# Performance work log

Hardware: AMD Instinct MI355X
Metric: run time of the kernel (lower is better)

The kernel has to match this reference:

```python
import jax, jax.numpy as jnp
import numpy as np

N_NODES = 50000


def _degrees(idx, n):
    d = jax.ops.segment_sum(jnp.ones(idx.shape, jnp.float32), idx, num_segments=n)
    return jnp.clip(d, 1.0)  # DGL clamps degree at 1


def gcn_layer(x, src, dst, W, b, n):
    """DGL GraphConv with norm='both': D_dst^-1/2 * sum_edges(D_src^-1/2 * x_src) @ W + b.
    Applies W before aggregation when in_feats > out_feats (cheaper), matching DGL."""
    inv_sqrt_out = _degrees(src, n) ** -0.5  # out-degree norm on source side
    inv_sqrt_in = _degrees(dst, n) ** -0.5   # in-degree norm on dest side
    h = x * inv_sqrt_out[:, None]
    if W.shape[0] > W.shape[1]:
        h = h @ W
        agg = jax.ops.segment_sum(h[src], dst, num_segments=n)
    else:
        agg = jax.ops.segment_sum(h[src], dst, num_segments=n)
        agg = agg @ W
    return agg * inv_sqrt_in[:, None] + b


def setup_inputs() -> dict:
    key = jax.random.key(0)
    ks = jax.random.split(key, 8)
    E = 800000
    in_feat = jax.random.normal(ks[0], (N_NODES, 1), dtype=jnp.float32)
    edge_index = jax.random.randint(ks[1], (2, E), 0, N_NODES, dtype=jnp.int32)
    def glorot(k, fan_in, fan_out):
        s = (6.0 / (fan_in + fan_out)) ** 0.5
        return jax.random.uniform(k, (fan_in, fan_out), jnp.float32, -s, s)
    W0 = glorot(ks[2], 1, 100); b0 = jnp.zeros((100,), jnp.float32)
    W1 = glorot(ks[3], 100, 10); b1 = jnp.zeros((10,), jnp.float32)
    W2 = glorot(ks[4], 10, 1); b2 = jnp.zeros((1,), jnp.float32)
    return {"in_feat": in_feat, "edge_index": edge_index,
            "W0": W0, "b0": b0, "W1": W1, "b1": b1, "W2": W2, "b2": b2}


def reference(in_feat, edge_index, W0, b0, W1, b1, W2, b2):
    src, dst = edge_index[0], edge_index[1]
    n = N_NODES
    h = gcn_layer(in_feat, src, dst, W0, b0, n)
    h = jax.nn.leaky_relu(h, negative_slope=0.01)
    h = gcn_layer(h, src, dst, W1, b1, n)
    h = jax.nn.relu(h)
    h = gcn_layer(h, src, dst, W2, b2, n)
    h = jax.nn.relu(h)
    return h
```

## Files before the change

kernel.cpp:

```cpp
#include <hip/hip_runtime.h>


#define NT 256
#define NTB 1024
#define K_BKT 250
#define R_NODES 200
#define SEG 48
#define CAP 4096
#define CHUNK 4096
#define BIN_BLOCKS 196
#define NSLOT (BIN_BLOCKS * SEG)
#define FINF 3.0e38f


__global__ __launch_bounds__(NT) void k_bin(const int4* __restrict__ src4,
                                            const int4* __restrict__ dst4, int E4,
                                            unsigned short* __restrict__ cntd16,
                                            unsigned short* __restrict__ cnts16,
                                            unsigned* __restrict__ dstSeg,
                                            unsigned short* __restrict__ srcSeg) {
  __shared__ unsigned cnt_d[K_BKT], cnt_s[K_BKT];
  int t = threadIdx.x, blk = blockIdx.x;
  for (int k = t; k < K_BKT; k += NT) { cnt_d[k] = 0u; cnt_s[k] = 0u; }
  __syncthreads();
  int base4 = blk * (CHUNK / 4);
  int4 sA[4], dA[4];
#pragma unroll
  for (int j = 0; j < 4; j++) {
    int e4 = base4 + j * NT + t;
    if (e4 < E4) { sA[j] = src4[e4]; dA[j] = dst4[e4]; }
    else { sA[j] = make_int4(-1, -1, -1, -1); dA[j] = make_int4(-1, -1, -1, -1); }
  }
  const int* sp = (const int*)sA;
  const int* dp = (const int*)dA;
#pragma unroll
  for (int j = 0; j < 16; j++) {
    int d = dp[j], s = sp[j];
    if (d >= 0) {
      unsigned bd = (unsigned)d / R_NODES;
      unsigned pd = atomicAdd(&cnt_d[bd], 1u);
      if (pd < SEG)
        dstSeg[((size_t)bd * BIN_BLOCKS + blk) * SEG + pd] =
            (unsigned)s | (((unsigned)d - bd * R_NODES) << 16);
      unsigned bs = (unsigned)s / R_NODES;
      unsigned ps = atomicAdd(&cnt_s[bs], 1u);
      if (ps < SEG)
        srcSeg[((size_t)bs * BIN_BLOCKS + blk) * SEG + ps] =
            (unsigned short)((unsigned)s - bs * R_NODES);
    }
  }
  __syncthreads();
  for (int k = t; k < K_BKT; k += NT) {
    unsigned cd = cnt_d[k]; if (cd > SEG) cd = SEG;
    unsigned cs = cnt_s[k]; if (cs > SEG) cs = SEG;
    cntd16[(size_t)blk * K_BKT + k] = (unsigned short)cd;
    cnts16[(size_t)blk * K_BKT + k] = (unsigned short)cs;
  }
}


struct BktLds {
  unsigned dslab[NSLOT];
  unsigned short sslab[NSLOT];
  unsigned cnt[R_NODES], cnts[R_NODES], cur[R_NODES];
  unsigned sc[256];
  unsigned short crow_d[256], crow_s[256];
  unsigned short stage[CAP];
};
struct PreLds {
  float W0s[100], b0s[100], W1s[1000];
  float beta[100], bsorted[128];
  int ord[100];
  float cA[1000], cB[1000];
  float baseA[16], baseB[16];
};
union BPool { BktLds b; PreLds p; };

__global__ __launch_bounds__(NTB) void k_bucket(
    const unsigned short* __restrict__ cntd16, const unsigned short* __restrict__ cnts16,
    const unsigned* __restrict__ dstSeg, const unsigned short* __restrict__ srcSeg,
    const float* __restrict__ x,
    const float* __restrict__ W0, const float* __restrict__ b0,
    const float* __restrict__ W1,
    float* __restrict__ betas, float* __restrict__ Aseg, float* __restrict__ Bseg,
    unsigned short* __restrict__ csr16,
    unsigned* __restrict__ rs, unsigned* __restrict__ rd,
    float* __restrict__ dsrc_inv, float* __restrict__ ddst_inv,
    float* __restrict__ s0, int n, int nbin) {
  __shared__ BPool u;
  int t = threadIdx.x, blk = blockIdx.x;
  if (blk < K_BKT) {
    const int b = blk;
    const int4* dsl4 = (const int4*)(dstSeg + (size_t)b * NSLOT);
    int4* dl4 = (int4*)u.b.dslab;
    for (int i = t; i < NSLOT / 4; i += NTB) dl4[i] = dsl4[i];
    const int4* ssl4 = (const int4*)(srcSeg + (size_t)b * NSLOT);
    int4* sl4 = (int4*)u.b.sslab;
    for (int i = t; i < NSLOT / 8; i += NTB) sl4[i] = ssl4[i];
    if (t < 256) {
      u.b.crow_d[t] = (t < nbin) ? cntd16[(size_t)t * K_BKT + b] : (unsigned short)0;
      u.b.crow_s[t] = (t < nbin) ? cnts16[(size_t)t * K_BKT + b] : (unsigned short)0;
    }
    for (int k = t; k < R_NODES; k += NTB) { u.b.cnt[k] = 0u; u.b.cnts[k] = 0u; }
    __syncthreads();
    for (int sl = t; sl < NSLOT; sl += NTB) {
      int blkI = sl / SEG, idx = sl - blkI * SEG;
      if (idx < (int)u.b.crow_d[blkI]) atomicAdd(&u.b.cnt[u.b.dslab[sl] >> 16], 1u);
      if (idx < (int)u.b.crow_s[blkI]) atomicAdd(&u.b.cnts[u.b.sslab[sl]], 1u);
    }
    __syncthreads();
    unsigned v = 0u;
    if (t < 256) {
      v = (t < R_NODES) ? u.b.cnt[t] : 0u;
      u.b.sc[t] = v;
    }
    __syncthreads();
    for (int off = 1; off < 256; off <<= 1) {
      unsigned a = (t >= off && t < 256) ? u.b.sc[t - off] : 0u;
      __syncthreads();
      if (t < 256) u.b.sc[t] += a;
      __syncthreads();
    }
    if (t < R_NODES) {
      unsigned st = u.b.sc[t] - v;
      int vg = b * R_NODES + t;
      if (vg < n) {
        unsigned di = u.b.cnt[t], dou = u.b.cnts[t];
        rs[vg] = (unsigned)b * CAP + st;
        rd[vg] = di;
        ddst_inv[vg] = rsqrtf((float)(di < 1u ? 1u : di));
        float ia = rsqrtf((float)(dou < 1u ? 1u : dou));
        dsrc_inv[vg] = ia;
        s0[vg] = x[vg] * ia;
      }
      u.b.cur[t] = st;
    }
    __syncthreads();
    for (int sl = t; sl < NSLOT; sl += NTB) {
      int blkI = sl / SEG, idx = sl - blkI * SEG;
      if (idx < (int)u.b.crow_d[blkI]) {
        unsigned e = u.b.dslab[sl];
        unsigned pos = atomicAdd(&u.b.cur[e >> 16], 1u);
        if (pos < CAP) u.b.stage[pos] = (unsigned short)(e & 0xFFFFu);
      }
    }
    __syncthreads();
    unsigned nd = u.b.sc[255]; if (nd > CAP) nd = CAP;
    int4* cg4 = (int4*)(csr16 + (size_t)b * CAP);
    const int4* st4 = (const int4*)u.b.stage;
    unsigned nv = (nd + 7) / 8;
    for (unsigned i = t; i < nv; i += NTB) cg4[i] = st4[i];
  } else {
    if (t < 100) { u.p.W0s[t] = W0[t]; u.p.b0s[t] = b0[t]; }
    for (int k = t; k < 1000; k += NTB) u.p.W1s[k] = W1[k];
    __syncthreads();
    if (t < 100) {
      float w = u.p.W0s[t];
      u.p.beta[t] = (w != 0.0f) ? (-u.p.b0s[t] / w) : FINF;
    }
    __syncthreads();
    if (t < 100) {
      float bt = u.p.beta[t];
      int r = 0;
      for (int j = 0; j < 100; j++) {
        float bj = u.p.beta[j];
        r += (bj < bt || (bj == bt && j < t)) ? 1 : 0;
      }
      u.p.bsorted[r] = bt;
      u.p.ord[r] = t;
    }
    if (t >= 100 && t < 128) u.p.bsorted[t] = FINF;
    __syncthreads();
    if (t < 128) betas[t] = u.p.bsorted[t];
    if (t < 1000) {
      int k = t / 10, j = t - k * 10;
      int f = u.p.ord[k];
      float w = u.p.W0s[f];
      float w1 = u.p.W1s[f * 10 + j];
      float ca = 0.0f, cb = 0.0f;
      if (w != 0.0f) {
        ca = 0.99f * fabsf(w) * w1;
        cb = 0.99f * ((w > 0.0f) ? 1.0f : -1.0f) * u.p.b0s[f] * w1;
      }
      u.p.cA[t] = ca;
      u.p.cB[t] = cb;
    }
    if (t < 10) {
      const int j = t;
      float a = 0.0f, bacc = 0.0f;
      for (int f = 0; f < 100; f++) {
        float w = u.p.W0s[f], bb = u.p.b0s[f], w1 = u.p.W1s[f * 10 + j];
        if (w == 0.0f) {
          float h = bb >= 0.0f ? bb : 0.01f * bb;
          bacc += h * w1;
        } else {
          float cc = (w > 0.0f) ? 0.01f : 1.0f;
          a += cc * w * w1;
          bacc += cc * bb * w1;
        }
      }
      Aseg[j] = a; Bseg[j] = bacc;
      u.p.baseA[j] = a; u.p.baseB[j] = bacc;
    }
    __syncthreads();
    for (int off = 1; off < 100; off <<= 1) {
      float a = 0.0f, bv = 0.0f;
      bool act = (t < 1000) && (t / 10 >= off);
      if (act) { a = u.p.cA[t - off * 10]; bv = u.p.cB[t - off * 10]; }
      __syncthreads();
      if (act) { u.p.cA[t] += a; u.p.cB[t] += bv; }
      __syncthreads();
    }
    if (t < 1000) {
      int k = t / 10, j = t - k * 10;
      Aseg[(k + 1) * 10 + j] = u.p.baseA[j] + u.p.cA[t];
      Bseg[(k + 1) * 10 + j] = u.p.baseB[j] + u.p.cB[t];
    }
  }
}


__global__ void k_g_l0l1(const unsigned* __restrict__ rs, const unsigned* __restrict__ rd,
                         const unsigned short* __restrict__ csr16,
                         const float* __restrict__ s0,
                         const float* __restrict__ dsrc_inv, const float* __restrict__ ddst_inv,
                         const float* __restrict__ betas,
                         float4* __restrict__ y4, int n) {
  __shared__ float bs_[128];
  for (int k = threadIdx.x; k < 128; k += blockDim.x) bs_[k] = betas[k];
  __syncthreads();
  int tid = blockIdx.x * blockDim.x + threadIdx.x;
  int v = tid >> 2, k4 = tid & 3;
  if (v >= n) return;
  unsigned base = rs[v], deg = rd[v];
  const unsigned short* row = csr16 + base;
  float c = 0.0f;
#pragma unroll 4
  for (unsigned i = k4; i < deg; i += 4) c += s0[row[i]];
  c += __shfl_xor(c, 1, 4);
  c += __shfl_xor(c, 2, 4);
  float c0 = c * ddst_inv[v];
  int lo = 0, hi = 100;
#pragma unroll
  for (int it = 0; it < 7; it++) {
    int mid = (lo + hi) >> 1;
    bool go = bs_[mid] < c0;
    lo = go ? mid + 1 : lo;
    hi = go ? hi : mid;
  }
  if (k4 == 0) {
    float so = dsrc_inv[v];
    y4[v] = make_float4(so * c0, so, __int_as_float(lo), 0.0f);
  }
}

__global__ void k_g10_l1l2(const unsigned* __restrict__ rs, const unsigned* __restrict__ rd,
                           const unsigned short* __restrict__ csr16,
                           const float4* __restrict__ y4,
                           const float* __restrict__ dsrc_inv, const float* __restrict__ ddst_inv,
                           const float* __restrict__ Aseg, const float* __restrict__ Bseg,
                           const float* __restrict__ b1, const float* __restrict__ W2,
                           float* __restrict__ t2, int n) {
  __shared__ float As[1010], Bs[1010];
  for (int k = threadIdx.x; k < 1010; k += blockDim.x) { As[k] = Aseg[k]; Bs[k] = Bseg[k]; }
  __syncthreads();
  int tid = blockIdx.x * blockDim.x + threadIdx.x;
  int v = tid >> 4, f = tid & 15;
  if (v >= n) return;
  unsigned base = rs[v], deg = rd[v];
  const unsigned short* row = csr16 + base;
  float acc = 0.0f;
  for (unsigned c = 0; c < deg; c += 16u) {
    unsigned i = c + (unsigned)f;
    int idx = (i < deg) ? (int)row[i] : 0;
    float4 y = y4[idx];
    unsigned m = deg - c; if (m > 16u) m = 16u;
    for (unsigned j = 0; j < m; j++) {
      float soc = __shfl(y.x, (int)j, 16);
      float so = __shfl(y.y, (int)j, 16);
      int sg = __shfl(__float_as_int(y.z), (int)j, 16);
      if (f < 10) {
        int o = sg * 10 + f;
        acc = fmaf(soc, As[o], acc);
        acc = fmaf(so, Bs[o], acc);
      }
    }
  }
  float p = 0.0f;
  if (f < 10) {
    float h = acc * ddst_inv[v] + b1[f];
    h = h > 0.0f ? h : 0.0f;
    p = h * W2[f];
  }
  p += __shfl_xor(p, 1, 16);
  p += __shfl_xor(p, 2, 16);
  p += __shfl_xor(p, 4, 16);
  p += __shfl_xor(p, 8, 16);
  if (f == 0) t2[v] = p * dsrc_inv[v];
}

__global__ void k_g_out(const unsigned* __restrict__ rs, const unsigned* __restrict__ rd,
                        const unsigned short* __restrict__ csr16,
                        const float* __restrict__ t2, const float* __restrict__ ddst_inv,
                        const float* __restrict__ b2, float* __restrict__ out, int n) {
  int tid = blockIdx.x * blockDim.x + threadIdx.x;
  int v = tid >> 2, k4 = tid & 3;
  if (v >= n) return;
  unsigned base = rs[v], deg = rd[v];
  const unsigned short* row = csr16 + base;
  float c = 0.0f;
#pragma unroll 4
  for (unsigned i = k4; i < deg; i += 4) c += t2[row[i]];
  c += __shfl_xor(c, 1, 4);
  c += __shfl_xor(c, 2, 4);
  if (k4 == 0) {
    float h = c * ddst_inv[v] + b2[0];
    out[v] = h > 0.0f ? h : 0.0f;
  }
}

extern "C" void kernel_launch(void* const* d_in, const int* in_sizes, int n_in,
                              void* d_out, int out_size, void* d_ws, size_t ws_size,
                              hipStream_t stream) {
  const float* in_feat = (const float*)d_in[0];
  const int* ei = (const int*)d_in[1];
  const float* W0 = (const float*)d_in[2];
  const float* b0 = (const float*)d_in[3];
  const float* W1 = (const float*)d_in[4];
  const float* b1 = (const float*)d_in[5];
  const float* W2 = (const float*)d_in[6];
  const float* b2 = (const float*)d_in[7];
  float* out = (float*)d_out;

  const int n = in_sizes[0];
  const int E = in_sizes[1] / 2;
  const int* src = ei;
  const int* dst = ei + E;
  const int E4 = E / 4;
  int nbin = (E + CHUNK - 1) / CHUNK;
  if (nbin > BIN_BLOCKS) nbin = BIN_BLOCKS;

  unsigned short* cntd16 = (unsigned short*)d_ws;
  unsigned short* cnts16 = cntd16 + (size_t)BIN_BLOCKS * K_BKT;
  unsigned* dstSeg = (unsigned*)(cnts16 + (size_t)BIN_BLOCKS * K_BKT);
  unsigned short* srcSeg = (unsigned short*)(dstSeg + (size_t)K_BKT * NSLOT);
  unsigned short* csr16 = srcSeg + (size_t)K_BKT * NSLOT;
  unsigned* rs = (unsigned*)(csr16 + (size_t)K_BKT * CAP + 64);
  unsigned* rd = rs + n;
  float* dsrc_inv = (float*)(rd + n);
  float* ddst_inv = dsrc_inv + n;
  float* s0 = ddst_inv + n;
  float4* y4 = (float4*)(s0 + n);
  float* t2 = (float*)(y4 + n);
  float* betas = t2 + n;
  float* Aseg = betas + 128;
  float* Bseg = Aseg + 1010;

  k_bin<<<nbin, NT, 0, stream>>>((const int4*)src, (const int4*)dst, E4,
                                 cntd16, cnts16, dstSeg, srcSeg);
  k_bucket<<<K_BKT + 1, NTB, 0, stream>>>(cntd16, cnts16, dstSeg, srcSeg, in_feat,
                                          W0, b0, W1, betas, Aseg, Bseg, csr16,
                                          rs, rd, dsrc_inv, ddst_inv, s0, n, nbin);
  k_g_l0l1<<<(4 * n + NT - 1) / NT, NT, 0, stream>>>(rs, rd, csr16, s0, dsrc_inv, ddst_inv,
                                                     betas, y4, n);
  k_g10_l1l2<<<(16 * n + NT - 1) / NT, NT, 0, stream>>>(rs, rd, csr16, y4, dsrc_inv, ddst_inv,
                                                        Aseg, Bseg, b1, W2, t2, n);
  k_g_out<<<(4 * n + NT - 1) / NT, NT, 0, stream>>>(rs, rd, csr16, t2, ddst_inv, b2, out, n);
}
```

Measured before the change: 61.36 us.

## Stage binned edges in LDS via counting sort for coalesced segment writes

The binning kernel now does a counting pass, an exclusive prefix scan over bucket counts, and then scatters edges into an LDS staging buffer sorted by bucket. It then writes them out to the per-bucket global segments in contiguous order, so the global stores are grouped instead of scattered. This adds an extra atomic pass, a scan with many barriers, and about 28KB of extra LDS per block, which may lower occupancy.

```diff
diff --git a/kernel.cpp b/kernel.cpp
--- a/kernel.cpp
+++ b/kernel.cpp
@@ -20,6 +20,12 @@
                                             unsigned* __restrict__ dstSeg,
                                             unsigned short* __restrict__ srcSeg) {
   __shared__ unsigned cnt_d[K_BKT], cnt_s[K_BKT];
+  __shared__ unsigned st_d[K_BKT], st_s[K_BKT];
+  __shared__ unsigned scd[NT], scs[NT];
+  __shared__ unsigned stg_d[CHUNK];
+  __shared__ unsigned short stgb_d[CHUNK];
+  __shared__ unsigned short stg_s[CHUNK];
+  __shared__ unsigned short stgb_s[CHUNK];
   int t = threadIdx.x, blk = blockIdx.x;
   for (int k = t; k < K_BKT; k += NT) { cnt_d[k] = 0u; cnt_s[k] = 0u; }
   __syncthreads();
@@ -35,24 +41,60 @@
   const int* dp = (const int*)dA;
 #pragma unroll
   for (int j = 0; j < 16; j++) {
+    if (dp[j] >= 0) {
+      atomicAdd(&cnt_d[(unsigned)dp[j] / R_NODES], 1u);
+      atomicAdd(&cnt_s[(unsigned)sp[j] / R_NODES], 1u);
+    }
+  }
+  __syncthreads();
+  unsigned vd = (t < K_BKT) ? cnt_d[t] : 0u;
+  unsigned vs = (t < K_BKT) ? cnt_s[t] : 0u;
+  scd[t] = vd; scs[t] = vs;
+  __syncthreads();
+  for (int off = 1; off < NT; off <<= 1) {
+    unsigned ad = (t >= off) ? scd[t - off] : 0u;
+    unsigned as = (t >= off) ? scs[t - off] : 0u;
+    __syncthreads();
+    scd[t] += ad; scs[t] += as;
+    __syncthreads();
+  }
+  if (t < K_BKT) {
+    st_d[t] = scd[t] - vd;
+    st_s[t] = scs[t] - vs;
+    cnt_d[t] = st_d[t];
+    cnt_s[t] = st_s[t];
+  }
+  __syncthreads();
+#pragma unroll
+  for (int j = 0; j < 16; j++) {
     int d = dp[j], s = sp[j];
     if (d >= 0) {
       unsigned bd = (unsigned)d / R_NODES;
       unsigned pd = atomicAdd(&cnt_d[bd], 1u);
-      if (pd < SEG)
-        dstSeg[((size_t)bd * BIN_BLOCKS + blk) * SEG + pd] =
-            (unsigned)s | (((unsigned)d - bd * R_NODES) << 16);
+      stg_d[pd] = (unsigned)s | (((unsigned)d - bd * R_NODES) << 16);
+      stgb_d[pd] = (unsigned short)bd;
       unsigned bs = (unsigned)s / R_NODES;
       unsigned ps = atomicAdd(&cnt_s[bs], 1u);
-      if (ps < SEG)
-        srcSeg[((size_t)bs * BIN_BLOCKS + blk) * SEG + ps] =
-            (unsigned short)((unsigned)s - bs * R_NODES);
-    }
-  }
-  __syncthreads();
+      stg_s[ps] = (unsigned short)((unsigned)s - bs * R_NODES);
+      stgb_s[ps] = (unsigned short)bs;
+    }
+  }
+  __syncthreads();
+  int total = E4 * 4 - blk * CHUNK;
+  if (total > CHUNK) total = CHUNK;
+  for (int j = t; j < total; j += NT) {
+    unsigned b = stgb_d[j];
+    unsigned off = (unsigned)j - st_d[b];
+    if (off < SEG) dstSeg[((size_t)b * BIN_BLOCKS + blk) * SEG + off] = stg_d[j];
+  }
+  for (int j = t; j < total; j += NT) {
+    unsigned b = stgb_s[j];
+    unsigned off = (unsigned)j - st_s[b];
+    if (off < SEG) srcSeg[((size_t)b * BIN_BLOCKS + blk) * SEG + off] = stg_s[j];
+  }
   for (int k = t; k < K_BKT; k += NT) {
-    unsigned cd = cnt_d[k]; if (cd > SEG) cd = SEG;
-    unsigned cs = cnt_s[k]; if (cs > SEG) cs = SEG;
+    unsigned cd = cnt_d[k] - st_d[k]; if (cd > SEG) cd = SEG;
+    unsigned cs = cnt_s[k] - st_s[k]; if (cs > SEG) cs = SEG;
     cntd16[(size_t)blk * K_BKT + k] = (unsigned short)cd;
     cnts16[(size_t)blk * K_BKT + k] = (unsigned short)cs;
   }
```

Measured after the change: 62.96 us. 2.6% more time.
